# Kernel tuning notes

Hardware: AMD Instinct MI355X
Metric: run time of the kernel (lower is better)

Reference implementation:

```python
import jax, jax.numpy as jnp
import numpy as np

N = 32768
H = 256

def setup_inputs() -> dict:
    key = jax.random.key(0)
    ks = jax.random.split(key, 8)
    def glorot(k, shape):
        fan_in, fan_out = shape
        s = jnp.sqrt(2.0 / (fan_in + fan_out)).astype(jnp.float32)
        return jax.random.normal(k, shape, dtype=jnp.float32) * s
    inp = {
        "x_norm": jax.random.normal(ks[0], (N, 3), dtype=jnp.float32),
        "nu": jnp.ones((1,), dtype=jnp.float32) * 0.01,
        "x_std": jnp.array([0.5, 0.5, 0.5], dtype=jnp.float32),
        "y_std": jnp.array([1.2, 1.2, 1.2, 0.8], dtype=jnp.float32),
        "W0": glorot(ks[1], (3, H)), "b0": jnp.zeros((H,), jnp.float32),
        "W1": glorot(ks[2], (H, H)), "b1": jnp.zeros((H,), jnp.float32),
        "W2": glorot(ks[3], (H, H)), "b2": jnp.zeros((H,), jnp.float32),
        "W3": glorot(ks[4], (H, H)), "b3": jnp.zeros((H,), jnp.float32),
        "W4": glorot(ks[5], (H, 4)), "b4": jnp.zeros((4,), jnp.float32),
    }
    return inp

def reference(x_norm, nu, x_std, y_std, W0, b0, W1, b1, W2, b2, W3, b3, W4, b4):
    # per-point MLP: R^3 -> R^4  (u, v, w, p)
    def f(x):
        h = jnp.tanh(x @ W0 + b0)
        h = jnp.tanh(h @ W1 + b1)
        h = jnp.tanh(h @ W2 + b2)
        h = jnp.tanh(h @ W3 + b3)
        return h @ W4 + b4  # [4]

    # Fused single-pass derivatives (replaces 13 autograd.grad calls):
    J = jax.vmap(jax.jacfwd(f))(x_norm)                 # [N,4,3] first derivs
    Hfull = jax.vmap(jax.jacfwd(jax.jacfwd(f)))(x_norm) # [N,4,3,3]
    Hdiag = jnp.diagonal(Hfull, axis1=2, axis2=3)       # [N,4,3] d2/dxi2 only

    # de-normalization scaling: y_std[y] / x_std[x]^order
    Js = J * y_std[None, :, None] / x_std[None, None, :]
    Hs = Hdiag * y_std[None, :, None] / (x_std[None, None, :] ** 2)

    continuity = Js[:, 0, 0] + Js[:, 1, 1] + Js[:, 2, 2]  # du/dx+dv/dy+dw/dz
    lap = Hs.sum(-1)                                       # [N,4] laplacians
    nu_s = nu[0]
    momentum_x = Js[:, 3, 0] - nu_s * lap[:, 0]
    momentum_y = Js[:, 3, 1] - nu_s * lap[:, 1]
    momentum_z = Js[:, 3, 2] - nu_s * lap[:, 2]

    phy_loss = continuity ** 2 + momentum_x ** 2 + momentum_y ** 2 + momentum_z ** 2
    return phy_loss  # [N], reduction='none' (already squeezed)
```

## Files before the change

### kernel.cpp

```cpp
#include <hip/hip_runtime.h>
#include <stdint.h>

typedef __attribute__((ext_vector_type(8))) _Float16 half8v;
typedef __attribute__((ext_vector_type(16))) float float16v;
typedef __attribute__((ext_vector_type(4))) float float4v;

#define NPTS_WG 32

__device__ __forceinline__ int agp(int c, int g, int p) {
    return ((c * 32 + g) * 32 + p) * 8;
}

__device__ __forceinline__ unsigned short f16b(float x) {
    const _Float16 h = (_Float16)x;
    return __builtin_bit_cast(unsigned short, h);
}

__device__ __forceinline__ uint32_t pk2f16(float a, float b) {
    return (uint32_t)f16b(a) | ((uint32_t)f16b(b) << 16);
}

__device__ __forceinline__ float fast_tanh(float z) {
    const float e = __expf(2.0f * z);
    return 1.0f - 2.0f / (e + 1.0f);
}

__global__ void wt_split_kernel(const float* __restrict__ W1, const float* __restrict__ W2,
                                const float* __restrict__ W3, unsigned short* __restrict__ wt)
{
    const int b = blockIdx.x;
    const int L = b >> 4;
    const int ch = b & 15;
    const int k0 = ch * 16;
    const float* W = (L == 0) ? W1 : (L == 1) ? W2 : W3;
    const int j = threadIdx.x;
    const int wv = j >> 5, l31 = j & 31;
    uint32_t hi[16], lo[16];
#pragma unroll
    for (int e = 0; e < 16; ++e) {
        const float x = W[(k0 + e) * 256 + j];
        const unsigned short h = f16b(x);
        const float hf = (float)__builtin_bit_cast(_Float16, h);
        hi[e] = h;
        lo[e] = f16b(x - hf);
    }
#pragma unroll
    for (int part = 0; part < 2; ++part) {
        const uint32_t* src = part ? lo : hi;
        unsigned short* base = wt +
            ((((size_t)(L * 2 + part) * 8 + wv) * 16 + ch) * 64) * 8;
#pragma unroll
        for (int hh = 0; hh < 2; ++hh) {
            uint4 v;
            const uint32_t* s = src + hh * 8;
            v.x = s[0] | (s[1] << 16);
            v.y = s[2] | (s[3] << 16);
            v.z = s[4] | (s[5] << 16);
            v.w = s[6] | (s[7] << 16);
            *(uint4*)(base + (hh * 32 + l31) * 8) = v;
        }
    }
}

__global__ __launch_bounds__(512, 2)
void pinn_mfma(const float* __restrict__ x_norm, const float* __restrict__ nu,
               const float* __restrict__ x_std, const float* __restrict__ y_std,
               const float* __restrict__ W0, const float* __restrict__ b0,
               const float* __restrict__ b1, const float* __restrict__ b2,
               const float* __restrict__ b3, const float* __restrict__ W4,
               const unsigned short* __restrict__ wt, float* __restrict__ out)
{
    __shared__ unsigned short AH[7 * 32 * 256];
    __shared__ float w4_lds[256 * 4];
    __shared__ float part_lds[8 * 6 * 32 * 4];
    __shared__ float y_lds[24 * 32];

    const int tid = threadIdx.x;
    const int lane = tid & 63;
    const int wv = tid >> 6;
    const int l31 = lane & 31;
    const int hh = lane >> 5;
    const int base_pt = blockIdx.x * NPTS_WG;

    if (tid < 256) ((float4*)w4_lds)[tid] = ((const float4*)W4)[tid];

    {
        const int p = tid & 31;
        const int jq = tid >> 5;
        const float x0 = x_norm[(base_pt + p) * 3 + 0];
        const float x1 = x_norm[(base_pt + p) * 3 + 1];
        const float x2 = x_norm[(base_pt + p) * 3 + 2];
#pragma unroll
        for (int hf = 0; hf < 2; ++hf) {
            const int j8 = jq * 16 + hf * 8;
            const int g = 2 * jq + hf;
            float w0r[8], w1r[8], w2r[8], b0r[8];
            *(float4*)&w0r[0] = *(const float4*)&W0[0 * 256 + j8];
            *(float4*)&w0r[4] = *(const float4*)&W0[0 * 256 + j8 + 4];
            *(float4*)&w1r[0] = *(const float4*)&W0[1 * 256 + j8];
            *(float4*)&w1r[4] = *(const float4*)&W0[1 * 256 + j8 + 4];
            *(float4*)&w2r[0] = *(const float4*)&W0[2 * 256 + j8];
            *(float4*)&w2r[4] = *(const float4*)&W0[2 * 256 + j8 + 4];
            *(float4*)&b0r[0] = *(const float4*)&b0[j8];
            *(float4*)&b0r[4] = *(const float4*)&b0[j8 + 4];
            union { unsigned short u[8]; half8v v; } hv[7];
#pragma unroll
            for (int e = 0; e < 8; ++e) {
                const float z = b0r[e] + x0 * w0r[e] + x1 * w1r[e] + x2 * w2r[e];
                const float t = fast_tanh(z);
                const float s = 1.f - t * t;
                hv[0].u[e] = f16b(t);
                const float wvv[3] = {w0r[e], w1r[e], w2r[e]};
#pragma unroll
                for (int i = 0; i < 3; ++i) {
                    hv[1 + i].u[e] = f16b(s * wvv[i]);
                    hv[4 + i].u[e] = f16b(-2.f * t * s * wvv[i] * wvv[i]);
                }
            }
#pragma unroll
            for (int c = 0; c < 7; ++c)
                *(half8v*)&AH[agp(c, g, p)] = hv[c].v;
        }
    }
    __syncthreads();

    const float* biases[3] = {b1, b2, b3};
    const int laneq = lane * 8;

#pragma unroll 1
    for (int L = 0; L < 3; ++L) {
        const unsigned short* whb = wt + (((size_t)(L * 2 + 0) * 8 + wv) * 16) * 512 + laneq;
        const unsigned short* wlb = wt + (((size_t)(L * 2 + 1) * 8 + wv) * 16) * 512 + laneq;
        float16v acc[7];
#pragma unroll
        for (int c = 0; c < 7; ++c)
#pragma unroll
            for (int e = 0; e < 16; ++e) acc[c][e] = 0.f;

        half8v wh[3], wl[3], a[7], na[7];
        wh[0] = *(const half8v*)(whb);
        wl[0] = *(const half8v*)(wlb);
        wh[1] = *(const half8v*)(whb + 512);
        wl[1] = *(const half8v*)(wlb + 512);
#pragma unroll
        for (int c = 0; c < 7; ++c)
            a[c] = *(const half8v*)&AH[agp(c, hh, l31)];

#pragma unroll
        for (int ch = 0; ch < 16; ++ch) {
            if (ch < 14) {
                wh[(ch + 2) % 3] = *(const half8v*)(whb + (ch + 2) * 512);
                wl[(ch + 2) % 3] = *(const half8v*)(wlb + (ch + 2) * 512);
            }
            if (ch < 15) {
                const int ng = 2 * (ch + 1) + hh;
#pragma unroll
                for (int c = 0; c < 7; ++c)
                    na[c] = *(const half8v*)&AH[agp(c, ng, l31)];
            }
            __builtin_amdgcn_s_setprio(1);
#pragma unroll
            for (int c = 0; c < 7; ++c) {
                acc[c] = __builtin_amdgcn_mfma_f32_32x32x16_f16(wh[ch % 3], a[c], acc[c], 0, 0, 0);
                if (c < 4)
                    acc[c] = __builtin_amdgcn_mfma_f32_32x32x16_f16(wl[ch % 3], a[c], acc[c], 0, 0, 0);
            }
            __builtin_amdgcn_s_setprio(0);
            if (ch < 15) {
#pragma unroll
                for (int c = 0; c < 7; ++c) a[c] = na[c];
            }
        }

        const float* bL = biases[L];
        __syncthreads();
#pragma unroll
        for (int q = 0; q < 4; ++q) {
            const int j0 = wv * 32 + 8 * q + 4 * hh;
            const int g = wv * 4 + q;
            float bj[4];
            *(float4*)&bj[0] = *(const float4*)&bL[j0];
            float val[7][4];
#pragma unroll
            for (int r = 0; r < 4; ++r) {
                const int e = q * 4 + r;
                const float z = acc[0][e] + bj[r];
                const float t = fast_tanh(z);
                const float s = 1.f - t * t;
                val[0][r] = t;
#pragma unroll
                for (int i = 0; i < 3; ++i) {
                    const float d1 = acc[1 + i][e];
                    const float d2 = acc[4 + i][e];
                    val[1 + i][r] = s * d1;
                    val[4 + i][r] = s * d2 - 2.f * t * s * d1 * d1;
                }
            }
#pragma unroll
            for (int c = 0; c < 7; ++c) {
                const uint32_t u0 = pk2f16(val[c][0], val[c][1]);
                const uint32_t u1 = pk2f16(val[c][2], val[c][3]);
                *(uint2*)&AH[agp(c, g, l31) + 4 * hh] = make_uint2(u0, u1);
            }
        }
        __syncthreads();
    }

    {
        const int l15 = lane & 15;
        const int g4 = lane >> 4;
        const int koct = wv * 32 + 8 * g4;
        const int gr = wv * 4 + g4;
        union { uint32_t u[4]; half8v v; } HB, LB;
#pragma unroll
        for (int i = 0; i < 4; ++i) {
            const float w0v = (l15 < 4) ? w4_lds[(koct + 2 * i) * 4 + l15] : 0.f;
            const float w1v = (l15 < 4) ? w4_lds[(koct + 2 * i + 1) * 4 + l15] : 0.f;
            const unsigned short h0 = f16b(w0v), h1 = f16b(w1v);
            const float r0 = w0v - (float)__builtin_bit_cast(_Float16, h0);
            const float r1 = w1v - (float)__builtin_bit_cast(_Float16, h1);
            HB.u[i] = (uint32_t)h0 | ((uint32_t)h1 << 16);
            LB.u[i] = (uint32_t)f16b(r0) | ((uint32_t)f16b(r1) << 16);
        }
        float4v acc4[6][2];
#pragma unroll
        for (int c = 0; c < 6; ++c)
#pragma unroll
            for (int ph = 0; ph < 2; ++ph) acc4[c][ph] = (float4v){0.f, 0.f, 0.f, 0.f};
#pragma unroll
        for (int c = 0; c < 6; ++c) {
#pragma unroll
            for (int ph = 0; ph < 2; ++ph) {
                const half8v ah = *(const half8v*)&AH[agp(1 + c, gr, l15 + 16 * ph)];
                acc4[c][ph] = __builtin_amdgcn_mfma_f32_16x16x32_f16(HB.v, ah, acc4[c][ph], 0, 0, 0);
                if (c < 3)
                    acc4[c][ph] = __builtin_amdgcn_mfma_f32_16x16x32_f16(LB.v, ah, acc4[c][ph], 0, 0, 0);
            }
        }
        if (g4 == 0) {
#pragma unroll
            for (int c = 0; c < 6; ++c)
#pragma unroll
                for (int ph = 0; ph < 2; ++ph)
                    *(float4*)&part_lds[((wv * 6 + c) * 32 + ph * 16 + l15) * 4] =
                        make_float4(acc4[c][ph][0], acc4[c][ph][1],
                                    acc4[c][ph][2], acc4[c][ph][3]);
        }
    }
    __syncthreads();

    {
        const int p = tid & 31;
#pragma unroll
        for (int co = tid >> 5; co < 24; co += 16) {
            const int o = co & 3;
            const int c6 = co >> 2;
            float sum = 0.f;
#pragma unroll
            for (int w8 = 0; w8 < 8; ++w8)
                sum += part_lds[((w8 * 6 + c6) * 32 + p) * 4 + o];
            const int i = (c6 < 3) ? c6 : (c6 - 3);
            const float xs = x_std[i];
            const float scale = y_std[o] / ((c6 < 3) ? xs : (xs * xs));
            y_lds[co * 32 + p] = sum * scale;
        }
    }
    __syncthreads();

    if (tid < 32) {
        const int p = tid;
        const float nuv = nu[0];
        #define YV(c6, o) y_lds[(((c6) * 4) + (o)) * 32 + p]
        const float cont = YV(0, 0) + YV(1, 1) + YV(2, 2);
        const float lap0 = YV(3, 0) + YV(4, 0) + YV(5, 0);
        const float lap1 = YV(3, 1) + YV(4, 1) + YV(5, 1);
        const float lap2 = YV(3, 2) + YV(4, 2) + YV(5, 2);
        const float mx = YV(0, 3) - nuv * lap0;
        const float my = YV(1, 3) - nuv * lap1;
        const float mz = YV(2, 3) - nuv * lap2;
        out[base_pt + p] = cont * cont + mx * mx + my * my + mz * mz;
        #undef YV
    }
}

extern "C" void kernel_launch(void* const* d_in, const int* in_sizes, int n_in,
                              void* d_out, int out_size, void* d_ws, size_t ws_size,
                              hipStream_t stream)
{
    const float* x_norm = (const float*)d_in[0];
    const float* nu     = (const float*)d_in[1];
    const float* x_std  = (const float*)d_in[2];
    const float* y_std  = (const float*)d_in[3];
    const float* W0 = (const float*)d_in[4];  const float* b0 = (const float*)d_in[5];
    const float* W1 = (const float*)d_in[6];  const float* b1 = (const float*)d_in[7];
    const float* W2 = (const float*)d_in[8];  const float* b2 = (const float*)d_in[9];
    const float* W3 = (const float*)d_in[10]; const float* b3 = (const float*)d_in[11];
    const float* W4 = (const float*)d_in[12];
    (void)n_in; (void)out_size; (void)ws_size;
    unsigned short* wt = (unsigned short*)d_ws;
    float* out = (float*)d_out;
    const int npts = in_sizes[0] / 3;

    wt_split_kernel<<<48, 256, 0, stream>>>(W1, W2, W3, wt);
    pinn_mfma<<<npts / NPTS_WG, 512, 0, stream>>>(x_norm, nu, x_std, y_std,
        W0, b0, b1, b2, b3, W4, wt, out);
}
```

Measured before the change: 172.0 us.

## Propagate scaled Laplacian as single channel and prefetch next layer operands

Replaces the three per-axis second-derivative channels with one channel carrying the x_std-weighted Laplacian, since only the sum is needed. This shrinks the propagated tangent channels from 7 to 5, cutting MFMA work, LDS footprint and the epilogue. The change also triple-buffers the activation loads and prefetches the next layer's first weight tiles and activations across the layer boundary. The cost is higher register pressure and a change in fp16 rounding order for the Laplacian term.

```diff
diff --git a/kernel.cpp b/kernel.cpp
--- a/kernel.cpp
+++ b/kernel.cpp
@@ -6,6 +6,7 @@
 typedef __attribute__((ext_vector_type(4))) float float4v;
 
 #define NPTS_WG 32
+#define NCH 5
 
 __device__ __forceinline__ int agp(int c, int g, int p) {
     return ((c * 32 + g) * 32 + p) * 8;
@@ -70,10 +71,10 @@
                const float* __restrict__ b3, const float* __restrict__ W4,
                const unsigned short* __restrict__ wt, float* __restrict__ out)
 {
-    __shared__ unsigned short AH[7 * 32 * 256];
+    __shared__ unsigned short AH[NCH * 32 * 256];
     __shared__ float w4_lds[256 * 4];
-    __shared__ float part_lds[8 * 6 * 32 * 4];
-    __shared__ float y_lds[24 * 32];
+    __shared__ float part_lds[8 * 4 * 32 * 4];
+    __shared__ float y_lds[16 * 32];
 
     const int tid = threadIdx.x;
     const int lane = tid & 63;
@@ -81,6 +82,11 @@
     const int l31 = lane & 31;
     const int hh = lane >> 5;
     const int base_pt = blockIdx.x * NPTS_WG;
+
+    const float xs0 = x_std[0], xs1 = x_std[1], xs2 = x_std[2];
+    const float ixs20 = 1.f / (xs0 * xs0);
+    const float ixs21 = 1.f / (xs1 * xs1);
+    const float ixs22 = 1.f / (xs2 * xs2);
 
     if (tid < 256) ((float4*)w4_lds)[tid] = ((const float4*)W4)[tid];
 
@@ -103,22 +109,22 @@
             *(float4*)&w2r[4] = *(const float4*)&W0[2 * 256 + j8 + 4];
             *(float4*)&b0r[0] = *(const float4*)&b0[j8];
             *(float4*)&b0r[4] = *(const float4*)&b0[j8 + 4];
-            union { unsigned short u[8]; half8v v; } hv[7];
+            union { unsigned short u[8]; half8v v; } hv[NCH];
 #pragma unroll
             for (int e = 0; e < 8; ++e) {
                 const float z = b0r[e] + x0 * w0r[e] + x1 * w1r[e] + x2 * w2r[e];
                 const float t = fast_tanh(z);
                 const float s = 1.f - t * t;
                 hv[0].u[e] = f16b(t);
-                const float wvv[3] = {w0r[e], w1r[e], w2r[e]};
-#pragma unroll
-                for (int i = 0; i < 3; ++i) {
-                    hv[1 + i].u[e] = f16b(s * wvv[i]);
-                    hv[4 + i].u[e] = f16b(-2.f * t * s * wvv[i] * wvv[i]);
-                }
-            }
-#pragma unroll
-            for (int c = 0; c < 7; ++c)
+                hv[1].u[e] = f16b(s * w0r[e]);
+                hv[2].u[e] = f16b(s * w1r[e]);
+                hv[3].u[e] = f16b(s * w2r[e]);
+                hv[4].u[e] = f16b(-2.f * t * s *
+                    (w0r[e] * w0r[e] * ixs20 + w1r[e] * w1r[e] * ixs21 +
+                     w2r[e] * w2r[e] * ixs22));
+            }
+#pragma unroll
+            for (int c = 0; c < NCH; ++c)
                 *(half8v*)&AH[agp(c, g, p)] = hv[c].v;
         }
     }
@@ -127,49 +133,57 @@
     const float* biases[3] = {b1, b2, b3};
     const int laneq = lane * 8;
 
+    const unsigned short* whb = wt + ((size_t)0 * 8 + wv) * 8192 + laneq;
+    const unsigned short* wlb = wt + ((size_t)1 * 8 + wv) * 8192 + laneq;
+
+    half8v wh[3], wl[3], ab[3][NCH];
+    wh[0] = *(const half8v*)(whb);
+    wl[0] = *(const half8v*)(wlb);
+    wh[1] = *(const half8v*)(whb + 512);
+    wl[1] = *(const half8v*)(wlb + 512);
+#pragma unroll
+    for (int c = 0; c < NCH; ++c) {
+        ab[0][c] = *(const half8v*)&AH[agp(c, hh, l31)];
+        ab[1][c] = *(const half8v*)&AH[agp(c, 2 + hh, l31)];
+    }
+
 #pragma unroll 1
     for (int L = 0; L < 3; ++L) {
-        const unsigned short* whb = wt + (((size_t)(L * 2 + 0) * 8 + wv) * 16) * 512 + laneq;
-        const unsigned short* wlb = wt + (((size_t)(L * 2 + 1) * 8 + wv) * 16) * 512 + laneq;
-        float16v acc[7];
-#pragma unroll
-        for (int c = 0; c < 7; ++c)
+        const unsigned short* whL = wt + ((size_t)(L * 2 + 0) * 8 + wv) * 8192 + laneq;
+        const unsigned short* wlL = wt + ((size_t)(L * 2 + 1) * 8 + wv) * 8192 + laneq;
+        float16v acc[NCH];
+#pragma unroll
+        for (int c = 0; c < NCH; ++c)
 #pragma unroll
             for (int e = 0; e < 16; ++e) acc[c][e] = 0.f;
-
-        half8v wh[3], wl[3], a[7], na[7];
-        wh[0] = *(const half8v*)(whb);
-        wl[0] = *(const half8v*)(wlb);
-        wh[1] = *(const half8v*)(whb + 512);
-        wl[1] = *(const half8v*)(wlb + 512);
-#pragma unroll
-        for (int c = 0; c < 7; ++c)
-            a[c] = *(const half8v*)&AH[agp(c, hh, l31)];
 
 #pragma unroll
         for (int ch = 0; ch < 16; ++ch) {
             if (ch < 14) {
-                wh[(ch + 2) % 3] = *(const half8v*)(whb + (ch + 2) * 512);
-                wl[(ch + 2) % 3] = *(const half8v*)(wlb + (ch + 2) * 512);
-            }
-            if (ch < 15) {
-                const int ng = 2 * (ch + 1) + hh;
-#pragma unroll
-                for (int c = 0; c < 7; ++c)
-                    na[c] = *(const half8v*)&AH[agp(c, ng, l31)];
+                wh[(ch + 2) % 3] = *(const half8v*)(whL + (ch + 2) * 512);
+                wl[(ch + 2) % 3] = *(const half8v*)(wlL + (ch + 2) * 512);
+                const int ng = 2 * (ch + 2) + hh;
+#pragma unroll
+                for (int c = 0; c < NCH; ++c)
+                    ab[(ch + 2) % 3][c] = *(const half8v*)&AH[agp(c, ng, l31)];
             }
             __builtin_amdgcn_s_setprio(1);
 #pragma unroll
-            for (int c = 0; c < 7; ++c) {
-                acc[c] = __builtin_amdgcn_mfma_f32_32x32x16_f16(wh[ch % 3], a[c], acc[c], 0, 0, 0);
-                if (c < 4)
-                    acc[c] = __builtin_amdgcn_mfma_f32_32x32x16_f16(wl[ch % 3], a[c], acc[c], 0, 0, 0);
-            }
+            for (int c = 0; c < NCH; ++c)
+                acc[c] = __builtin_amdgcn_mfma_f32_32x32x16_f16(wh[ch % 3], ab[ch % 3][c], acc[c], 0, 0, 0);
+#pragma unroll
+            for (int c = 0; c < 4; ++c)
+                acc[c] = __builtin_amdgcn_mfma_f32_32x32x16_f16(wl[ch % 3], ab[ch % 3][c], acc[c], 0, 0, 0);
             __builtin_amdgcn_s_setprio(0);
-            if (ch < 15) {
-#pragma unroll
-                for (int c = 0; c < 7; ++c) a[c] = na[c];
-            }
+        }
+
+        if (L < 2) {
+            const unsigned short* whN = wt + ((size_t)((L + 1) * 2 + 0) * 8 + wv) * 8192 + laneq;
+            const unsigned short* wlN = wt + ((size_t)((L + 1) * 2 + 1) * 8 + wv) * 8192 + laneq;
+            wh[0] = *(const half8v*)(whN);
+            wl[0] = *(const half8v*)(wlN);
+            wh[1] = *(const half8v*)(whN + 512);
+            wl[1] = *(const half8v*)(wlN + 512);
         }
 
         const float* bL = biases[L];
@@ -180,30 +194,36 @@
             const int g = wv * 4 + q;
             float bj[4];
             *(float4*)&bj[0] = *(const float4*)&bL[j0];
-            float val[7][4];
+            float val[NCH][4];
 #pragma unroll
             for (int r = 0; r < 4; ++r) {
                 const int e = q * 4 + r;
                 const float z = acc[0][e] + bj[r];
                 const float t = fast_tanh(z);
                 const float s = 1.f - t * t;
+                const float d1a = acc[1][e], d1b = acc[2][e], d1c = acc[3][e];
                 val[0][r] = t;
-#pragma unroll
-                for (int i = 0; i < 3; ++i) {
-                    const float d1 = acc[1 + i][e];
-                    const float d2 = acc[4 + i][e];
-                    val[1 + i][r] = s * d1;
-                    val[4 + i][r] = s * d2 - 2.f * t * s * d1 * d1;
-                }
-            }
-#pragma unroll
-            for (int c = 0; c < 7; ++c) {
+                val[1][r] = s * d1a;
+                val[2][r] = s * d1b;
+                val[3][r] = s * d1c;
+                val[4][r] = s * acc[4][e] - 2.f * t * s *
+                    (d1a * d1a * ixs20 + d1b * d1b * ixs21 + d1c * d1c * ixs22);
+            }
+#pragma unroll
+            for (int c = 0; c < NCH; ++c) {
                 const uint32_t u0 = pk2f16(val[c][0], val[c][1]);
                 const uint32_t u1 = pk2f16(val[c][2], val[c][3]);
                 *(uint2*)&AH[agp(c, g, l31) + 4 * hh] = make_uint2(u0, u1);
             }
         }
         __syncthreads();
+        if (L < 2) {
+#pragma unroll
+            for (int c = 0; c < NCH; ++c) {
+                ab[0][c] = *(const half8v*)&AH[agp(c, hh, l31)];
+                ab[1][c] = *(const half8v*)&AH[agp(c, 2 + hh, l31)];
+            }
+        }
     }
 
     {
@@ -222,62 +242,55 @@
             HB.u[i] = (uint32_t)h0 | ((uint32_t)h1 << 16);
             LB.u[i] = (uint32_t)f16b(r0) | ((uint32_t)f16b(r1) << 16);
         }
-        float4v acc4[6][2];
-#pragma unroll
-        for (int c = 0; c < 6; ++c)
-#pragma unroll
-            for (int ph = 0; ph < 2; ++ph) acc4[c][ph] = (float4v){0.f, 0.f, 0.f, 0.f};
-#pragma unroll
-        for (int c = 0; c < 6; ++c) {
+        float4v acc4[4][2];
+#pragma unroll
+        for (int cc = 0; cc < 4; ++cc)
+#pragma unroll
+            for (int ph = 0; ph < 2; ++ph) acc4[cc][ph] = (float4v){0.f, 0.f, 0.f, 0.f};
+#pragma unroll
+        for (int cc = 0; cc < 4; ++cc) {
 #pragma unroll
             for (int ph = 0; ph < 2; ++ph) {
-                const half8v ah = *(const half8v*)&AH[agp(1 + c, gr, l15 + 16 * ph)];
-                acc4[c][ph] = __builtin_amdgcn_mfma_f32_16x16x32_f16(HB.v, ah, acc4[c][ph], 0, 0, 0);
-                if (c < 3)
-                    acc4[c][ph] = __builtin_amdgcn_mfma_f32_16x16x32_f16(LB.v, ah, acc4[c][ph], 0, 0, 0);
+                const half8v ah = *(const half8v*)&AH[agp(1 + cc, gr, l15 + 16 * ph)];
+                acc4[cc][ph] = __builtin_amdgcn_mfma_f32_16x16x32_f16(HB.v, ah, acc4[cc][ph], 0, 0, 0);
+                if (cc < 3)
+                    acc4[cc][ph] = __builtin_amdgcn_mfma_f32_16x16x32_f16(LB.v, ah, acc4[cc][ph], 0, 0, 0);
             }
         }
         if (g4 == 0) {
 #pragma unroll
-            for (int c = 0; c < 6; ++c)
+            for (int cc = 0; cc < 4; ++cc)
 #pragma unroll
                 for (int ph = 0; ph < 2; ++ph)
-                    *(float4*)&part_lds[((wv * 6 + c) * 32 + ph * 16 + l15) * 4] =
-                        make_float4(acc4[c][ph][0], acc4[c][ph][1],
-                                    acc4[c][ph][2], acc4[c][ph][3]);
+                    *(float4*)&part_lds[((wv * 4 + cc) * 32 + ph * 16 + l15) * 4] =
+                        make_float4(acc4[cc][ph][0], acc4[cc][ph][1],
+                                    acc4[cc][ph][2], acc4[cc][ph][3]);
         }
     }
     __syncthreads();
 
     {
         const int p = tid & 31;
-#pragma unroll
-        for (int co = tid >> 5; co < 24; co += 16) {
-            const int o = co & 3;
-            const int c6 = co >> 2;
-            float sum = 0.f;
-#pragma unroll
-            for (int w8 = 0; w8 < 8; ++w8)
-                sum += part_lds[((w8 * 6 + c6) * 32 + p) * 4 + o];
-            const int i = (c6 < 3) ? c6 : (c6 - 3);
-            const float xs = x_std[i];
-            const float scale = y_std[o] / ((c6 < 3) ? xs : (xs * xs));
-            y_lds[co * 32 + p] = sum * scale;
-        }
+        const int co = tid >> 5;
+        const int o = co & 3;
+        const int c4 = co >> 2;
+        float sum = 0.f;
+#pragma unroll
+        for (int w8 = 0; w8 < 8; ++w8)
+            sum += part_lds[((w8 * 4 + c4) * 32 + p) * 4 + o];
+        const float scale = (c4 < 3) ? (y_std[o] / x_std[c4]) : y_std[o];
+        y_lds[co * 32 + p] = sum * scale;
     }
     __syncthreads();
 
     if (tid < 32) {
         const int p = tid;
         const float nuv = nu[0];
-        #define YV(c6, o) y_lds[(((c6) * 4) + (o)) * 32 + p]
+        #define YV(c4, o) y_lds[(((c4) * 4) + (o)) * 32 + p]
         const float cont = YV(0, 0) + YV(1, 1) + YV(2, 2);
-        const float lap0 = YV(3, 0) + YV(4, 0) + YV(5, 0);
-        const float lap1 = YV(3, 1) + YV(4, 1) + YV(5, 1);
-        const float lap2 = YV(3, 2) + YV(4, 2) + YV(5, 2);
-        const float mx = YV(0, 3) - nuv * lap0;
-        const float my = YV(1, 3) - nuv * lap1;
-        const float mz = YV(2, 3) - nuv * lap2;
+        const float mx = YV(0, 3) - nuv * YV(3, 0);
+        const float my = YV(1, 3) - nuv * YV(3, 1);
+        const float mz = YV(2, 3) - nuv * YV(3, 2);
         out[base_pt + p] = cont * cont + mx * mx + my * my + mz * mz;
         #undef YV
     }
```

Measured after the change: 146.4 us (median of 2 runs). 14.9% less time.
